# Kernel tuning notes

Measured on AMD Instinct MI355X. Metric: run time of the kernel, lower is better.

Reference implementation:

```python
import jax, jax.numpy as jnp
import numpy as np

BN_EPS = 1e-5
TAU = 1.0

def _conv(x, w, pad, groups=1):
    return jax.lax.conv_general_dilated(
        x, w, (1, 1), [(pad, pad), (pad, pad)],
        feature_group_count=groups,
        dimension_numbers=('NCHW', 'OIHW', 'NCHW'))

def _bn(x, p):
    # p: (4, C) rows = gamma, beta, running_mean, running_var (eval-mode BN)
    g, b, m, v = p[0], p[1], p[2], p[3]
    scale = g * jax.lax.rsqrt(v + BN_EPS)
    shift = b - m * scale
    return x * scale[None, :, None, None] + shift[None, :, None, None]

def _dsconv(x, dw, bn1, pw, bn2, pad):
    c = x.shape[1]
    h = jax.nn.silu(_bn(_conv(x, dw, pad, groups=c), bn1))
    return jax.nn.silu(_bn(_conv(h, pw, 0), bn2))

def _make_bn(key, ch):
    k1, k2, k3, k4 = jax.random.split(key, 4)
    g = 1.0 + 0.1 * jax.random.normal(k1, (ch,), jnp.float32)
    b = 0.1 * jax.random.normal(k2, (ch,), jnp.float32)
    m = 0.1 * jax.random.normal(k3, (ch,), jnp.float32)
    v = 0.5 + jax.random.uniform(k4, (ch,), jnp.float32)
    return jnp.stack([g, b, m, v])

def setup_inputs() -> dict:
    key = jax.random.key(0)
    ks = jax.random.split(key, 18)
    B, C, H, W = 4, 256, 128, 128
    P, K = 64, 8
    inp = {
        'x':      jax.random.normal(ks[0], (B, C, H, W), jnp.float32),
        'fp_w1':  0.05 * jax.random.normal(ks[1], (P, C, 1, 1), jnp.float32),
        'fp_bn1': _make_bn(ks[2], P),
        'fp_dw':  0.2 * jax.random.normal(ks[3], (P, 1, 3, 3), jnp.float32),
        'fp_bn2': _make_bn(ks[4], P),
        'protos': jax.random.normal(ks[5], (K, P), jnp.float32),
        'bs_dw':  0.2 * jax.random.normal(ks[6], (1, 1, 3, 3), jnp.float32),
        'bs_bn1': _make_bn(ks[7], 1),
        'bs_pw':  0.2 * jax.random.normal(ks[8], (8, 1, 1, 1), jnp.float32),
        'bs_bn2': _make_bn(ks[9], 8),
        'bl_dw':  0.2 * jax.random.normal(ks[10], (1, 1, 5, 5), jnp.float32),
        'bl_bn1': _make_bn(ks[11], 1),
        'bl_pw':  0.2 * jax.random.normal(ks[12], (8, 1, 1, 1), jnp.float32),
        'bl_bn2': _make_bn(ks[13], 8),
        'fuse_w': 0.2 * jax.random.normal(ks[14], (1, 16, 1, 1), jnp.float32),
        'fuse_b': 0.1 * jax.random.normal(ks[15], (1,), jnp.float32),
        'gamma':  0.5 * jax.random.normal(ks[16], (1,), jnp.float32),
    }
    return inp

def reference(x, fp_w1, fp_bn1, fp_dw, fp_bn2, protos,
              bs_dw, bs_bn1, bs_pw, bs_bn2,
              bl_dw, bl_bn1, bl_pw, bl_bn2,
              fuse_w, fuse_b, gamma):
    # feature_proj: 1x1 conv -> BN -> SiLU -> depthwise 3x3 -> BN -> SiLU
    h = jax.nn.silu(_bn(_conv(x, fp_w1, 0), fp_bn1))
    proj = jax.nn.silu(_bn(_conv(h, fp_dw, 1, groups=fp_dw.shape[0]), fp_bn2))

    # deviation: min L2 distance to K bg prototypes, per-image min-max normalized
    B, P, H, W = proj.shape
    feat = proj.reshape(B, P, H * W).transpose(0, 2, 1)      # (B, HW, P)
    d2 = ((feat * feat).sum(-1, keepdims=True)               # (B, HW, 1)
          + (protos * protos).sum(-1)                        # (K,)
          - 2.0 * jnp.einsum('bnp,kp->bnk', feat, protos))   # (B, HW, K)
    dist = jnp.sqrt(jnp.maximum(d2, 0.0))
    min_dist = dist.min(axis=2) / (TAU + 1e-6)               # (B, HW)
    d_min = min_dist.min(axis=1, keepdims=True)
    d_max = min_dist.max(axis=1, keepdims=True)
    deviation = ((min_dist - d_min) / (d_max - d_min + 1e-6)).reshape(B, 1, H, W)

    # deviation -> attention head: two DS-conv branches (3x3 and 5x5), fuse 1x1, sigmoid
    f1 = _dsconv(deviation, bs_dw, bs_bn1, bs_pw, bs_bn2, pad=1)
    f2 = _dsconv(deviation, bl_dw, bl_bn1, bl_pw, bl_bn2, pad=2)
    attn = jax.nn.sigmoid(_conv(jnp.concatenate([f1, f2], axis=1), fuse_w, 0)
                          + fuse_b[None, :, None, None])
    return x + gamma * (x * attn)
```

## Files before the change

### kernel.cpp

```cpp
#include <hip/hip_runtime.h>
#include <math.h>

#define C_IN 256
#define P_CH 64
#define H_IMG 128
#define W_IMG 128
#define HW (H_IMG*W_IMG)
#define N_IMG 4
#define K_PROTO 8
#define BN_EPS 1e-5f

typedef unsigned short u16;
typedef __attribute__((ext_vector_type(4))) short bf16x4;
typedef __attribute__((ext_vector_type(8))) short bf16x8;
typedef __attribute__((ext_vector_type(4))) float f32x4;

#define OFF_H    0
#define OFF_MD   2097152
#define OFF_BMM  (2097152 + 65536)

__device__ __forceinline__ float silu_f(float x) { return x / (1.f + __expf(-x)); }

__device__ __forceinline__ u16 f2bf(float f) {
    union { float f; unsigned u; } v; v.f = f;
    unsigned r = v.u + 0x7fffu + ((v.u >> 16) & 1u);
    return (u16)(r >> 16);
}
__device__ __forceinline__ float bf2f(u16 s) {
    union { unsigned u; float f; } v; v.u = ((unsigned)s) << 16; return v.f;
}

#define LDA 36
#define LDB 264
__global__ __launch_bounds__(256) void conv1x1_kernel(
    const float* __restrict__ x, const float* __restrict__ w1,
    const float* __restrict__ bn1, u16* __restrict__ h)
{
    __shared__ u16 As[2][128 * LDA];
    __shared__ u16 Bs[64 * LDB];
    __shared__ float bias_s[64];
    int bx = blockIdx.x;
    int img = bx >> 7, row = bx & 127;
    int tid = threadIdx.x;
    int wid = tid >> 6, lane = tid & 63;
    int mm = lane & 15, kb = lane >> 4;

    {
        int n = tid >> 2, k0 = (tid & 3) * 64;
        float sc = bn1[n] * rsqrtf(bn1[192 + n] + BN_EPS);
        if ((tid & 3) == 0) bias_s[n] = bn1[64 + n] - bn1[128 + n] * sc;
        const float* src = w1 + n * 256 + k0;
        u16* dst = Bs + n * LDB + k0;
#pragma unroll
        for (int i = 0; i < 64; i += 4) {
            float4 v = *(const float4*)(src + i);
            ushort4 o;
            o.x = f2bf(v.x * sc); o.y = f2bf(v.y * sc);
            o.z = f2bf(v.z * sc); o.w = f2bf(v.w * sc);
            *(ushort4*)(dst + i) = o;
        }
    }

    int cp = tid >> 4, pg = tid & 15;
    const float* xbase = x + (size_t)img * C_IN * HW + row * W_IMG;
    {
        const float* xc0 = xbase + (size_t)(2 * cp) * HW;
        const float* xc1 = xc0 + HW;
#pragma unroll
        for (int i = 0; i < 8; ++i) {
            int px = pg + 16 * i;
            ushort2 pk; pk.x = f2bf(xc0[px]); pk.y = f2bf(xc1[px]);
            *(ushort2*)(&As[0][px * LDA + 2 * cp]) = pk;
        }
    }
    __syncthreads();

    f32x4 acc[2][4];
#pragma unroll
    for (int mt = 0; mt < 2; ++mt)
#pragma unroll
        for (int nt = 0; nt < 4; ++nt) acc[mt][nt] = (f32x4){0.f, 0.f, 0.f, 0.f};

    for (int k = 0; k < 8; ++k) {
        float p0[8], p1[8];
        if (k < 7) {
            const float* xc0 = xbase + (size_t)((k + 1) * 32 + 2 * cp) * HW;
            const float* xc1 = xc0 + HW;
#pragma unroll
            for (int i = 0; i < 8; ++i) {
                int px = pg + 16 * i;
                p0[i] = xc0[px]; p1[i] = xc1[px];
            }
        }

        const u16* Ab = As[k & 1];
        bf16x8 afrag[2], bfrag[4];
#pragma unroll
        for (int mt = 0; mt < 2; ++mt) {
            const u16* ap = Ab + (wid * 32 + mt * 16 + mm) * LDA + kb * 8;
            bf16x4 lo = *(const bf16x4*)ap;
            bf16x4 hi = *(const bf16x4*)(ap + 4);
            afrag[mt] = __builtin_shufflevector(lo, hi, 0, 1, 2, 3, 4, 5, 6, 7);
        }
#pragma unroll
        for (int nt = 0; nt < 4; ++nt)
            bfrag[nt] = *(const bf16x8*)(Bs + (nt * 16 + mm) * LDB + k * 32 + kb * 8);
#pragma unroll
        for (int mt = 0; mt < 2; ++mt)
#pragma unroll
            for (int nt = 0; nt < 4; ++nt)
                acc[mt][nt] = __builtin_amdgcn_mfma_f32_16x16x32_bf16(
                    afrag[mt], bfrag[nt], acc[mt][nt], 0, 0, 0);

        if (k < 7) {
            u16* An = As[(k + 1) & 1];
#pragma unroll
            for (int i = 0; i < 8; ++i) {
                int px = pg + 16 * i;
                ushort2 pk; pk.x = f2bf(p0[i]); pk.y = f2bf(p1[i]);
                *(ushort2*)(&An[px * LDA + 2 * cp]) = pk;
            }
        }
        __syncthreads();
    }

#pragma unroll
    for (int mt = 0; mt < 2; ++mt) {
        int pxb = wid * 32 + mt * 16 + kb * 4;
#pragma unroll
        for (int nt = 0; nt < 4; ++nt) {
            int n = nt * 16 + mm;
            float bb = bias_s[n];
            ushort4 o;
            o.x = f2bf(silu_f(acc[mt][nt][0] + bb));
            o.y = f2bf(silu_f(acc[mt][nt][1] + bb));
            o.z = f2bf(silu_f(acc[mt][nt][2] + bb));
            o.w = f2bf(silu_f(acc[mt][nt][3] + bb));
            *(ushort4*)(h + ((size_t)img * P_CH + n) * HW + row * W_IMG + pxb) = o;
        }
    }
}

__global__ __launch_bounds__(1024) void dwconv_dev_kernel(
    const u16* __restrict__ h, const float* __restrict__ dw,
    const float* __restrict__ bn2, const float* __restrict__ protos,
    float* __restrict__ md, float* __restrict__ bmm)
{
    __shared__ float smem[4 * 8 * 324];
    __shared__ float pnorm_s[K_PROTO];
    int img = blockIdx.x >> 6;
    int t = blockIdx.x & 63;
    int y0 = (t >> 3) << 4, x0 = (t & 7) << 4;
    int tid = threadIdx.x;
    int q = tid >> 8;
    int qtid = tid & 255;
    int ty = qtid >> 4, tx = qtid & 15;

    if (tid < K_PROTO) {
        const float4* pr = (const float4*)(protos + tid * 64);
        float s = 0.f;
#pragma unroll
        for (int i = 0; i < 16; ++i) {
            float4 v = pr[i];
            s += v.x * v.x + v.y * v.y + v.z * v.z + v.w * v.w;
        }
        pnorm_s[tid] = s;
    }

    const u16* himg = h + (size_t)img * P_CH * HW;
    float* qt = smem + q * (8 * 324);

    int  pre_off[11];
    bool pre_ok[11];
    bool pre_v[11];
#pragma unroll
    for (int r = 0; r < 11; ++r) {
        int l = qtid + r * 256;
        bool valid = l < 2592;
        int cl = l / 324;
        int rr = l - cl * 324;
        int ly = rr / 18, lx = rr - ly * 18;
        int yy = y0 - 1 + ly, xx = x0 - 1 + lx;
        bool inb = (yy >= 0) & (yy < H_IMG) & (xx >= 0) & (xx < W_IMG);
        pre_v[r] = valid;
        pre_ok[r] = valid && inb;
        pre_off[r] = cl * HW + (inb ? (yy * W_IMG + xx) : 0);
    }

    float norm2 = 0.f;
    float dot[K_PROTO];
#pragma unroll
    for (int k = 0; k < K_PROTO; ++k) dot[k] = 0.f;

    {
        const u16* hs = himg + (size_t)(q * 16) * HW;
#pragma unroll
        for (int r = 0; r < 11; ++r) {
            float v = pre_ok[r] ? bf2f(hs[pre_off[r]]) : 0.f;
            if (pre_v[r]) qt[qtid + r * 256] = v;
        }
    }
    __syncthreads();

    for (int k = 0; k < 2; ++k) {
        float pf[11];
        if (k == 0) {
            const u16* hs = himg + (size_t)(q * 16 + 8) * HW;
#pragma unroll
            for (int r = 0; r < 11; ++r)
                pf[r] = pre_ok[r] ? bf2f(hs[pre_off[r]]) : 0.f;
        }

        int c0 = q * 16 + k * 8;
#pragma unroll
        for (int cl = 0; cl < 8; ++cl) {
            int ch = c0 + cl;
            const float* tc = qt + cl * 324;
            const float* wch = dw + ch * 9;
            float s = 0.f;
#pragma unroll
            for (int dy = 0; dy < 3; ++dy)
#pragma unroll
                for (int dx = 0; dx < 3; ++dx)
                    s = fmaf(tc[(ty + dy) * 18 + tx + dx], wch[dy * 3 + dx], s);
            float g = bn2[ch], bb = bn2[64 + ch], m = bn2[128 + ch], vv = bn2[192 + ch];
            float scale = g * rsqrtf(vv + BN_EPS);
            float val = silu_f(scale * s + (bb - m * scale));
            norm2 = fmaf(val, val, norm2);
#pragma unroll
            for (int kk = 0; kk < K_PROTO; ++kk)
                dot[kk] = fmaf(val, protos[kk * 64 + ch], dot[kk]);
        }

        if (k == 0) {
            __syncthreads();
#pragma unroll
            for (int r = 0; r < 11; ++r)
                if (pre_v[r]) qt[qtid + r * 256] = pf[r];
            __syncthreads();
        }
    }
    __syncthreads();

    float* P = smem;
    {
        float* dst = P + (q * 256 + qtid) * 9;
        dst[0] = norm2;
#pragma unroll
        for (int kk = 0; kk < K_PROTO; ++kk) dst[1 + kk] = dot[kk];
    }
    __syncthreads();

    float wmin = 1e30f, wmax = -1e30f, mdv = 0.f;
    if (q == 0) {
        float n2 = 0.f, dd[K_PROTO];
#pragma unroll
        for (int kk = 0; kk < K_PROTO; ++kk) dd[kk] = 0.f;
#pragma unroll
        for (int qq = 0; qq < 4; ++qq) {
            const float* src = P + (qq * 256 + qtid) * 9;
            n2 += src[0];
#pragma unroll
            for (int kk = 0; kk < K_PROTO; ++kk) dd[kk] += src[1 + kk];
        }
        float d2min = 1e30f;
#pragma unroll
        for (int kk = 0; kk < K_PROTO; ++kk)
            d2min = fminf(d2min, n2 + pnorm_s[kk] - 2.f * dd[kk]);
        mdv = sqrtf(fmaxf(d2min, 0.f)) * (1.f / 1.000001f);
        md[img * HW + (y0 + ty) * W_IMG + (x0 + tx)] = mdv;
        wmin = mdv; wmax = mdv;
#pragma unroll
        for (int d = 32; d > 0; d >>= 1) {
            wmin = fminf(wmin, __shfl_xor(wmin, d));
            wmax = fmaxf(wmax, __shfl_xor(wmax, d));
        }
    }
    __syncthreads();
    if (q == 0 && (qtid & 63) == 0) {
        int wid = qtid >> 6;
        smem[wid * 2]     = wmin;
        smem[wid * 2 + 1] = wmax;
    }
    __syncthreads();
    if (tid == 0) {
        float bmin = fminf(fminf(smem[0], smem[2]), fminf(smem[4], smem[6]));
        float bmax = fmaxf(fmaxf(smem[1], smem[3]), fmaxf(smem[5], smem[7]));
        bmm[(img * 64 + t) * 2]     = bmin;
        bmm[(img * 64 + t) * 2 + 1] = bmax;
    }
}

__global__ __launch_bounds__(256) void attn_final_kernel(
    const float* __restrict__ x, const float* __restrict__ md,
    const float* __restrict__ bmm,
    const float* __restrict__ bs_dw, const float* __restrict__ bs_bn1,
    const float* __restrict__ bs_pw, const float* __restrict__ bs_bn2,
    const float* __restrict__ bl_dw, const float* __restrict__ bl_bn1,
    const float* __restrict__ bl_pw, const float* __restrict__ bl_bn2,
    const float* __restrict__ fuse_w, const float* __restrict__ fuse_b,
    const float* __restrict__ gamma, float* __restrict__ out)
{
    __shared__ float tile[20 * 20];
    __shared__ __align__(16) float attn_s[256];
    __shared__ float mmred[2];
    int bx = blockIdx.x;
    int img = bx >> 8;
    int t = (bx >> 2) & 63;
    int cg = bx & 3;
    int y0 = (t >> 3) << 4, x0 = (t & 7) << 4;
    int tid = threadIdx.x;
    int ty = tid >> 4, tx = tid & 15;

    if (tid < 64) {
        float mn = bmm[(img * 64 + tid) * 2];
        float mx = bmm[(img * 64 + tid) * 2 + 1];
#pragma unroll
        for (int d = 32; d > 0; d >>= 1) {
            mn = fminf(mn, __shfl_xor(mn, d));
            mx = fmaxf(mx, __shfl_xor(mx, d));
        }
        if (tid == 0) { mmred[0] = mn; mmred[1] = mx; }
    }
    __syncthreads();

    float fdmin = mmred[0];
    float fdmax = mmred[1];
    float inv = 1.f / (fdmax - fdmin + 1e-6f);

    const float* mdi = md + img * HW;
    for (int l = tid; l < 400; l += 256) {
        int ly = l / 20, lx = l - ly * 20;
        int yy = y0 - 2 + ly, xx = x0 - 2 + lx;
        float v = 0.f;
        if (yy >= 0 && yy < H_IMG && xx >= 0 && xx < W_IMG)
            v = (mdi[yy * W_IMG + xx] - fdmin) * inv;
        tile[l] = v;
    }
    __syncthreads();

    float c3 = 0.f;
#pragma unroll
    for (int dy = 0; dy < 3; ++dy)
#pragma unroll
        for (int dx = 0; dx < 3; ++dx)
            c3 = fmaf(tile[(ty + 1 + dy) * 20 + tx + 1 + dx], bs_dw[dy * 3 + dx], c3);
    float c5 = 0.f;
#pragma unroll
    for (int dy = 0; dy < 5; ++dy)
#pragma unroll
        for (int dx = 0; dx < 5; ++dx)
            c5 = fmaf(tile[(ty + dy) * 20 + tx + dx], bl_dw[dy * 5 + dx], c5);

    float s1 = bs_bn1[0] * rsqrtf(bs_bn1[3] + BN_EPS);
    float t1 = silu_f(s1 * c3 + (bs_bn1[1] - bs_bn1[2] * s1));
    float s2 = bl_bn1[0] * rsqrtf(bl_bn1[3] + BN_EPS);
    float t2 = silu_f(s2 * c5 + (bl_bn1[1] - bl_bn1[2] * s2));

    float acc = fuse_b[0];
#pragma unroll
    for (int c = 0; c < 8; ++c) {
        float scs = bs_bn2[c] * rsqrtf(bs_bn2[24 + c] + BN_EPS);
        float u1 = silu_f(scs * (bs_pw[c] * t1) + (bs_bn2[8 + c] - bs_bn2[16 + c] * scs));
        acc = fmaf(fuse_w[c], u1, acc);
        float scl = bl_bn2[c] * rsqrtf(bl_bn2[24 + c] + BN_EPS);
        float u2 = silu_f(scl * (bl_pw[c] * t2) + (bl_bn2[8 + c] - bl_bn2[16 + c] * scl));
        acc = fmaf(fuse_w[8 + c], u2, acc);
    }
    attn_s[tid] = 1.f / (1.f + __expf(-acc));
    __syncthreads();

    int j = tid & 63, cs = tid >> 6;
    int yy = y0 + (j >> 2), xq = x0 + (j & 3) * 4;
    float4 am = *(const float4*)&attn_s[(j >> 2) * 16 + (j & 3) * 4];
    float g = gamma[0];
    float m0 = 1.f + g * am.x, m1 = 1.f + g * am.y;
    float m2 = 1.f + g * am.z, m3 = 1.f + g * am.w;
    size_t base = ((size_t)(img * C_IN + cg * 64 + cs * 16)) * HW
                + (size_t)yy * W_IMG + xq;
#pragma unroll
    for (int c = 0; c < 16; ++c) {
        const float4 xv = *(const float4*)(x + base + (size_t)c * HW);
        float4 o;
        o.x = xv.x * m0; o.y = xv.y * m1; o.z = xv.z * m2; o.w = xv.w * m3;
        *(float4*)(out + base + (size_t)c * HW) = o;
    }
}

extern "C" void kernel_launch(void* const* d_in, const int* in_sizes, int n_in,
                              void* d_out, int out_size, void* d_ws, size_t ws_size,
                              hipStream_t stream) {
    const float* x      = (const float*)d_in[0];
    const float* fp_w1  = (const float*)d_in[1];
    const float* fp_bn1 = (const float*)d_in[2];
    const float* fp_dw  = (const float*)d_in[3];
    const float* fp_bn2 = (const float*)d_in[4];
    const float* protos = (const float*)d_in[5];
    const float* bs_dw  = (const float*)d_in[6];
    const float* bs_bn1 = (const float*)d_in[7];
    const float* bs_pw  = (const float*)d_in[8];
    const float* bs_bn2 = (const float*)d_in[9];
    const float* bl_dw  = (const float*)d_in[10];
    const float* bl_bn1 = (const float*)d_in[11];
    const float* bl_pw  = (const float*)d_in[12];
    const float* bl_bn2 = (const float*)d_in[13];
    const float* fuse_w = (const float*)d_in[14];
    const float* fuse_b = (const float*)d_in[15];
    const float* gamma  = (const float*)d_in[16];
    float* ws  = (float*)d_ws;
    float* out = (float*)d_out;

    conv1x1_kernel<<<512, 256, 0, stream>>>(x, fp_w1, fp_bn1, (u16*)(ws + OFF_H));
    dwconv_dev_kernel<<<256, 1024, 0, stream>>>((const u16*)(ws + OFF_H), fp_dw, fp_bn2,
                                                protos, ws + OFF_MD, ws + OFF_BMM);
    attn_final_kernel<<<1024, 256, 0, stream>>>(x, ws + OFF_MD, ws + OFF_BMM,
                                                bs_dw, bs_bn1, bs_pw, bs_bn2,
                                                bl_dw, bl_bn1, bl_pw, bl_bn2,
                                                fuse_w, fuse_b, gamma, out);
}
```

Before: 192.7 us.

## Vectorize conv1x1 x loads and split attention from final streaming kernel

The conv1x1 staging now has each thread load float4 rows from one channel instead of scalar loads from two channels. The bf16 values are then scattered into the transposed LDS tile with strided 16-bit stores. The old attention-plus-scale kernel is split in two. One kernel computes the per-pixel attention map once into workspace, and a second flat elementwise kernel streams x and writes out with fully contiguous float4 accesses. This removes the fourfold recomputation of the attention head per tile and improves coalescing, at the cost of an extra launch, an attention-map round trip through memory, and possible LDS bank conflicts from the 2-byte scatter stores.

```diff
diff --git a/kernel.cpp b/kernel.cpp
--- a/kernel.cpp
+++ b/kernel.cpp
@@ -6,7 +6,6 @@
 #define H_IMG 128
 #define W_IMG 128
 #define HW (H_IMG*W_IMG)
-#define N_IMG 4
 #define K_PROTO 8
 #define BN_EPS 1e-5f
 
@@ -18,6 +17,7 @@
 #define OFF_H    0
 #define OFF_MD   2097152
 #define OFF_BMM  (2097152 + 65536)
+#define OFF_ATTN (OFF_BMM + 512)
 
 __device__ __forceinline__ float silu_f(float x) { return x / (1.f + __expf(-x)); }
 
@@ -61,16 +61,19 @@
         }
     }
 
-    int cp = tid >> 4, pg = tid & 15;
+    int sch = tid >> 3, sq = tid & 7;
     const float* xbase = x + (size_t)img * C_IN * HW + row * W_IMG;
     {
-        const float* xc0 = xbase + (size_t)(2 * cp) * HW;
-        const float* xc1 = xc0 + HW;
-#pragma unroll
-        for (int i = 0; i < 8; ++i) {
-            int px = pg + 16 * i;
-            ushort2 pk; pk.x = f2bf(xc0[px]); pk.y = f2bf(xc1[px]);
-            *(ushort2*)(&As[0][px * LDA + 2 * cp]) = pk;
+        const float* xc = xbase + (size_t)sch * HW;
+#pragma unroll
+        for (int i = 0; i < 4; ++i) {
+            int px0 = sq * 4 + i * 32;
+            float4 v = *(const float4*)(xc + px0);
+            u16* d = &As[0][px0 * LDA + sch];
+            d[0]       = f2bf(v.x);
+            d[LDA]     = f2bf(v.y);
+            d[2 * LDA] = f2bf(v.z);
+            d[3 * LDA] = f2bf(v.w);
         }
     }
     __syncthreads();
@@ -82,15 +85,12 @@
         for (int nt = 0; nt < 4; ++nt) acc[mt][nt] = (f32x4){0.f, 0.f, 0.f, 0.f};
 
     for (int k = 0; k < 8; ++k) {
-        float p0[8], p1[8];
+        float4 pf[4];
         if (k < 7) {
-            const float* xc0 = xbase + (size_t)((k + 1) * 32 + 2 * cp) * HW;
-            const float* xc1 = xc0 + HW;
-#pragma unroll
-            for (int i = 0; i < 8; ++i) {
-                int px = pg + 16 * i;
-                p0[i] = xc0[px]; p1[i] = xc1[px];
-            }
+            const float* xc = xbase + (size_t)((k + 1) * 32 + sch) * HW;
+#pragma unroll
+            for (int i = 0; i < 4; ++i)
+                pf[i] = *(const float4*)(xc + sq * 4 + i * 32);
         }
 
         const u16* Ab = As[k & 1];
@@ -115,10 +115,13 @@
         if (k < 7) {
             u16* An = As[(k + 1) & 1];
 #pragma unroll
-            for (int i = 0; i < 8; ++i) {
-                int px = pg + 16 * i;
-                ushort2 pk; pk.x = f2bf(p0[i]); pk.y = f2bf(p1[i]);
-                *(ushort2*)(&An[px * LDA + 2 * cp]) = pk;
+            for (int i = 0; i < 4; ++i) {
+                int px0 = sq * 4 + i * 32;
+                u16* d = &An[px0 * LDA + sch];
+                d[0]       = f2bf(pf[i].x);
+                d[LDA]     = f2bf(pf[i].y);
+                d[2 * LDA] = f2bf(pf[i].z);
+                d[3 * LDA] = f2bf(pf[i].w);
             }
         }
         __syncthreads();
@@ -251,7 +254,7 @@
     }
     __syncthreads();
 
-    float wmin = 1e30f, wmax = -1e30f, mdv = 0.f;
+    float wmin = 1e30f, wmax = -1e30f;
     if (q == 0) {
         float n2 = 0.f, dd[K_PROTO];
 #pragma unroll
@@ -267,7 +270,7 @@
 #pragma unroll
         for (int kk = 0; kk < K_PROTO; ++kk)
             d2min = fminf(d2min, n2 + pnorm_s[kk] - 2.f * dd[kk]);
-        mdv = sqrtf(fmaxf(d2min, 0.f)) * (1.f / 1.000001f);
+        float mdv = sqrtf(fmaxf(d2min, 0.f)) * (1.f / 1.000001f);
         md[img * HW + (y0 + ty) * W_IMG + (x0 + tx)] = mdv;
         wmin = mdv; wmax = mdv;
 #pragma unroll
@@ -278,9 +281,9 @@
     }
     __syncthreads();
     if (q == 0 && (qtid & 63) == 0) {
-        int wid = qtid >> 6;
-        smem[wid * 2]     = wmin;
-        smem[wid * 2 + 1] = wmax;
+        int wd = qtid >> 6;
+        smem[wd * 2]     = wmin;
+        smem[wd * 2 + 1] = wmax;
     }
     __syncthreads();
     if (tid == 0) {
@@ -291,23 +294,19 @@
     }
 }
 
-__global__ __launch_bounds__(256) void attn_final_kernel(
-    const float* __restrict__ x, const float* __restrict__ md,
-    const float* __restrict__ bmm,
+__global__ __launch_bounds__(256) void attn_kernel(
+    const float* __restrict__ md, const float* __restrict__ bmm,
     const float* __restrict__ bs_dw, const float* __restrict__ bs_bn1,
     const float* __restrict__ bs_pw, const float* __restrict__ bs_bn2,
     const float* __restrict__ bl_dw, const float* __restrict__ bl_bn1,
     const float* __restrict__ bl_pw, const float* __restrict__ bl_bn2,
     const float* __restrict__ fuse_w, const float* __restrict__ fuse_b,
-    const float* __restrict__ gamma, float* __restrict__ out)
+    float* __restrict__ attn)
 {
     __shared__ float tile[20 * 20];
-    __shared__ __align__(16) float attn_s[256];
     __shared__ float mmred[2];
-    int bx = blockIdx.x;
-    int img = bx >> 8;
-    int t = (bx >> 2) & 63;
-    int cg = bx & 3;
+    int img = blockIdx.x >> 6;
+    int t = blockIdx.x & 63;
     int y0 = (t >> 3) << 4, x0 = (t & 7) << 4;
     int tid = threadIdx.x;
     int ty = tid >> 4, tx = tid & 15;
@@ -325,8 +324,7 @@
     __syncthreads();
 
     float fdmin = mmred[0];
-    float fdmax = mmred[1];
-    float inv = 1.f / (fdmax - fdmin + 1e-6f);
+    float inv = 1.f / (mmred[1] - fdmin + 1e-6f);
 
     const float* mdi = md + img * HW;
     for (int l = tid; l < 400; l += 256) {
@@ -367,23 +365,28 @@
         float u2 = silu_f(scl * (bl_pw[c] * t2) + (bl_bn2[8 + c] - bl_bn2[16 + c] * scl));
         acc = fmaf(fuse_w[8 + c], u2, acc);
     }
-    attn_s[tid] = 1.f / (1.f + __expf(-acc));
-    __syncthreads();
-
-    int j = tid & 63, cs = tid >> 6;
-    int yy = y0 + (j >> 2), xq = x0 + (j & 3) * 4;
-    float4 am = *(const float4*)&attn_s[(j >> 2) * 16 + (j & 3) * 4];
+    attn[img * HW + (y0 + ty) * W_IMG + (x0 + tx)] = 1.f / (1.f + __expf(-acc));
+}
+
+__global__ __launch_bounds__(256) void final_kernel(
+    const float* __restrict__ x, const float* __restrict__ attn,
+    const float* __restrict__ gamma, float* __restrict__ out)
+{
     float g = gamma[0];
-    float m0 = 1.f + g * am.x, m1 = 1.f + g * am.y;
-    float m2 = 1.f + g * am.z, m3 = 1.f + g * am.w;
-    size_t base = ((size_t)(img * C_IN + cg * 64 + cs * 16)) * HW
-                + (size_t)yy * W_IMG + xq;
-#pragma unroll
-    for (int c = 0; c < 16; ++c) {
-        const float4 xv = *(const float4*)(x + base + (size_t)c * HW);
+    size_t f4 = (size_t)blockIdx.x * 256 + threadIdx.x;
+#pragma unroll
+    for (int c = 0; c < 4; ++c) {
+        size_t i = (f4 + (size_t)c * 1048576) * 4;
+        int img_i = (int)(i >> 22);
+        int hw    = (int)(i & (size_t)(HW - 1));
+        float4 av = *(const float4*)(attn + ((size_t)img_i << 14) + hw);
+        float4 xv = *(const float4*)(x + i);
         float4 o;
-        o.x = xv.x * m0; o.y = xv.y * m1; o.z = xv.z * m2; o.w = xv.w * m3;
-        *(float4*)(out + base + (size_t)c * HW) = o;
+        o.x = xv.x * (1.f + g * av.x);
+        o.y = xv.y * (1.f + g * av.y);
+        o.z = xv.z * (1.f + g * av.z);
+        o.w = xv.w * (1.f + g * av.w);
+        *(float4*)(out + i) = o;
     }
 }
 
@@ -413,8 +416,9 @@
     conv1x1_kernel<<<512, 256, 0, stream>>>(x, fp_w1, fp_bn1, (u16*)(ws + OFF_H));
     dwconv_dev_kernel<<<256, 1024, 0, stream>>>((const u16*)(ws + OFF_H), fp_dw, fp_bn2,
                                                 protos, ws + OFF_MD, ws + OFF_BMM);
-    attn_final_kernel<<<1024, 256, 0, stream>>>(x, ws + OFF_MD, ws + OFF_BMM,
-                                                bs_dw, bs_bn1, bs_pw, bs_bn2,
-                                                bl_dw, bl_bn1, bl_pw, bl_bn2,
-                                                fuse_w, fuse_b, gamma, out);
-}
+    attn_kernel<<<256, 256, 0, stream>>>(ws + OFF_MD, ws + OFF_BMM,
+                                         bs_dw, bs_bn1, bs_pw, bs_bn2,
+                                         bl_dw, bl_bn1, bl_pw, bl_bn2,
+                                         fuse_w, fuse_b, ws + OFF_ATTN);
+    final_kernel<<<4096, 256, 0, stream>>>(x, ws + OFF_ATTN, gamma, out);
+}
```

After: 184.7 us. 4.2% less time.
